# Optimization experiments

Measured on AMD Instinct MI355X. Metric: run time of the kernel, lower is better.

The kernel has to match this reference:

```python
import jax, jax.numpy as jnp
import numpy as np
from jax import lax

N, C, H, W = 16, 512, 64, 64
INTER, HEADS, GROUPS, K = 512, 64, 8, 7
HEAD_DIM = INTER // HEADS


def setup_inputs() -> dict:
    key = jax.random.key(0)
    ks = jax.random.split(key, 12)
    s = 0.02
    return {
        "x": jax.random.normal(ks[0], (N, C, H, W), jnp.float32),
        "conv_w": jax.random.normal(ks[1], (INTER, C // GROUPS, K, K), jnp.float32) * s,
        "conv_b": jax.random.normal(ks[2], (INTER,), jnp.float32) * s,
        "ln_g": jnp.ones((INTER,), jnp.float32),
        "ln_b": jnp.zeros((INTER,), jnp.float32),
        "qw": jax.random.normal(ks[3], (INTER, INTER), jnp.float32) * s,
        "qb": jax.random.normal(ks[4], (INTER,), jnp.float32) * s,
        "kw": jax.random.normal(ks[5], (INTER, INTER), jnp.float32) * s,
        "kb": jax.random.normal(ks[6], (INTER,), jnp.float32) * s,
        "vw": jax.random.normal(ks[7], (INTER, INTER), jnp.float32) * s,
        "vb": jax.random.normal(ks[8], (INTER,), jnp.float32) * s,
        "pw": jax.random.normal(ks[9], (C, INTER), jnp.float32) * s,
        "pb": jax.random.normal(ks[10], (C,), jnp.float32) * s,
        "beta": jax.random.normal(ks[11], (1,), jnp.float32),
    }


def reference(x, conv_w, conv_b, ln_g, ln_b, qw, qb, kw, kb, vw, vb, pw, pb, beta):
    n, c, h, w = x.shape
    hw = h * w
    pad = (K - 1) // 2
    # grouped conv, NCHW
    xc = lax.conv_general_dilated(
        x, conv_w, window_strides=(1, 1), padding=[(pad, pad), (pad, pad)],
        dimension_numbers=("NCHW", "OIHW", "NCHW"), feature_group_count=GROUPS)
    xc = xc + conv_b[None, :, None, None]
    xc = xc.reshape(n, INTER, hw).transpose(0, 2, 1)  # [N, HW, INTER]
    # LayerNorm over channel dim
    mu = jnp.mean(xc, axis=-1, keepdims=True)
    var = jnp.mean(jnp.square(xc - mu), axis=-1, keepdims=True)
    xn = (xc - mu) * lax.rsqrt(var + 1e-5) * ln_g + ln_b
    # projections (torch Linear: y = x @ W.T + b)
    q = (xn @ qw.T + qb).reshape(n, hw, HEADS, HEAD_DIM).transpose(0, 2, 1, 3)  # [N,h,HW,d]
    k = (xn @ kw.T + kb).reshape(n, hw, HEADS, HEAD_DIM).transpose(0, 2, 3, 1)  # [N,h,d,HW]
    v = (xn @ vw.T + vb).reshape(n, hw, HEADS, HEAD_DIM).transpose(0, 2, 1, 3)  # [N,h,HW,d]
    k = jax.nn.softmax(k, axis=3)  # softmax over tokens
    corr = jnp.einsum("nhds,nhse->nhde", k, v)      # [N,h,d,d] compact context
    atten = jnp.einsum("nhsd,nhde->nhse", q, corr)  # [N,h,HW,d]
    atten = atten.transpose(0, 2, 1, 3).reshape(n, hw, INTER)
    xa = (atten @ pw.T + pb).transpose(0, 2, 1).reshape(n, c, h, w)
    return beta[0] * xa + x
```

## Files before the change

kernel.cpp:

```cpp
#include <hip/hip_runtime.h>
#include <hip/hip_bf16.h>

#define N_IMG 16
#define C_DIM 512
#define H_DIM 64
#define W_DIM 64
#define HW 4096
#define INTER 512
#define HEADS 64
#define GROUPS 8
#define KSZ 7
#define CPG 64
#define M_TOT (N_IMG * HW)

typedef short bf16x8 __attribute__((ext_vector_type(8)));
typedef short bf16x4 __attribute__((ext_vector_type(4)));
typedef float f32x4 __attribute__((ext_vector_type(4)));
typedef unsigned int u32;

__device__ __forceinline__ unsigned short f2bf(float f) {
    __hip_bfloat16 h = __float2bfloat16(f);
    return *reinterpret_cast<unsigned short*>(&h);
}
__device__ __forceinline__ float bf2f(unsigned short u) {
    u32 x = ((u32)u) << 16;
    union { u32 i; float f; } c; c.i = x; return c.f;
}
__device__ __forceinline__ void gload16(const void* g, void* l) {
    __builtin_amdgcn_global_load_lds(
        (const __attribute__((address_space(1))) u32*)g,
        (__attribute__((address_space(3))) u32*)l, 16, 0, 0);
}

__global__ __launch_bounds__(256) void zero_kernel(float* __restrict__ p)
{
    p[blockIdx.x * 256 + threadIdx.x] = 0.f;
}

__global__ __launch_bounds__(256) void wpack_kernel(
    const float* __restrict__ cw, unsigned short* __restrict__ pk)
{
    int p = blockIdx.x * 256 + threadIdx.x;
    int ci = p & 63;
    int co = (p >> 6) & 63;
    int r  = p >> 12;
    int dx = r % 7;
    int dyg = r / 7;
    int dy = dyg % 7;
    int g  = dyg / 7;
    float v = cw[(((size_t)(g * 64 + co)) * 64 + ci) * 49 + dy * 7 + dx];
    pk[(size_t)(g * 49 + dy * 7 + dx) * 4096 + co * 64 + (ci ^ ((co & 7) << 3))] = f2bf(v);
}

__global__ __launch_bounds__(256) void wpack_proj_kernel(
    const float* __restrict__ w, unsigned short* __restrict__ wp)
{
    int e = blockIdx.x * 256 + threadIdx.x;
    int j = e & 7;
    int chunk = (e >> 3) & 511;
    int kt = (e >> 12) & 15;
    int t = e >> 16;
    int col = chunk & 127, kq = chunk >> 7;
    wp[e] = f2bf(w[(size_t)(t * 128 + col) * 512 + kt * 32 + kq * 8 + j]);
}

__global__ __launch_bounds__(256) void xprep_kernel(
    const float* __restrict__ x, unsigned short* __restrict__ xb)
{
    const int row = blockIdx.x;
    const int g   = blockIdx.y;
    const int n   = blockIdx.z;
    const int tid = threadIdx.x;
    unsigned short* dst = xb + ((size_t)(n * 8 + g) * 70 + row) * 4608;

    if (row < 3 || row > 66) {
        bf16x8 z = (bf16x8){0,0,0,0,0,0,0,0};
        *(bf16x8*)&dst[tid * 8] = z;
        *(bf16x8*)&dst[(256 + tid) * 8] = z;
        if (tid < 64) *(bf16x8*)&dst[(512 + tid) * 8] = z;
        return;
    }
    const int y = row - 3;
    const int xcol = tid & 63;
    const int oct = tid >> 6;
    const int col = xcol + 3;
    const int cswz = (col & 7) << 3;
    const float* src = x + (((size_t)(n * C_DIM + g * CPG)) * H_DIM + y) * W_DIM + xcol;
#pragma unroll
    for (int h = 0; h < 2; ++h) {
        const int ci0 = oct * 16 + h * 8;
        unsigned short tmp[8];
#pragma unroll
        for (int j = 0; j < 8; ++j)
            tmp[j] = f2bf(src[(size_t)(ci0 + j) * (H_DIM * W_DIM)]);
        *(bf16x8*)&dst[col * 64 + (ci0 ^ cswz)] = *(bf16x8*)tmp;
    }
    if (tid < 64) {
        const int hc[8] = {0, 1, 2, 67, 68, 69, 70, 71};
        int c = hc[tid >> 3], o8 = (tid & 7) * 8;
        *(bf16x8*)&dst[c * 64 + (o8 ^ ((c & 7) << 3))] = (bf16x8){0,0,0,0,0,0,0,0};
    }
}

__global__ __launch_bounds__(256) void conv_mfma2_kernel(
    const unsigned short* __restrict__ xb, const unsigned short* __restrict__ pk,
    const float* __restrict__ cb, unsigned short* __restrict__ xc)
{
    __shared__ __align__(16) unsigned short in_ring[4 * 72 * 64];
    __shared__ __align__(16) unsigned short w_lds[2 * 4096];

    const int bid  = blockIdx.x;
    const int wgid = (bid & 7) * 256 + (bid >> 3);
    const int g  = wgid >> 8;
    const int n  = (wgid >> 4) & 15;
    const int y0 = (wgid & 15) * 4;
    const int tid  = threadIdx.x;
    const int lane = tid & 63;
    const int wv   = tid >> 6;
    const int lx   = lane & 15;
    const int q4   = lane >> 4;
    const int koff = q4 * 8;

    const unsigned short* xbase = xb + ((size_t)(n * 8 + g) * 70) * 4608;
    const unsigned short* pkg   = pk + (size_t)g * 49 * 4096;

    f32x4 acc[4][4];
#pragma unroll
    for (int i = 0; i < 4; ++i)
#pragma unroll
        for (int j = 0; j < 4; ++j) acc[i][j] = (f32x4){0.f, 0.f, 0.f, 0.f};

#pragma unroll
    for (int r = 0; r < 4; ++r) {
        const unsigned short* src = xbase + (size_t)(y0 + r) * 4608;
        gload16(src + tid * 8,         &in_ring[r * 4608 + tid * 8]);
        gload16(src + (256 + tid) * 8, &in_ring[r * 4608 + (256 + tid) * 8]);
        if (tid < 64)
            gload16(src + (512 + tid) * 8, &in_ring[r * 4608 + (512 + tid) * 8]);
    }
    gload16(pkg + tid * 8,         &w_lds[tid * 8]);
    gload16(pkg + (256 + tid) * 8, &w_lds[(256 + tid) * 8]);
    __syncthreads();

    for (int dy = 0; dy < 7; ++dy) {
        if (dy > 0) {
            const int slot = (dy + 3) & 3;
            const unsigned short* src = xbase + (size_t)(y0 + dy + 3) * 4608;
            gload16(src + tid * 8,         &in_ring[slot * 4608 + tid * 8]);
            gload16(src + (256 + tid) * 8, &in_ring[slot * 4608 + (256 + tid) * 8]);
            if (tid < 64)
                gload16(src + (512 + tid) * 8, &in_ring[slot * 4608 + (512 + tid) * 8]);
            __syncthreads();
        }
#pragma unroll
        for (int dx = 0; dx < 7; ++dx) {
            const int t = dy * 7 + dx;
            if (t < 48) {
                const unsigned short* wsrc = pkg + (size_t)(t + 1) * 4096;
                unsigned short* wdst = &w_lds[((t + 1) & 1) * 4096];
                gload16(wsrc + tid * 8,         wdst + tid * 8);
                gload16(wsrc + (256 + tid) * 8, wdst + (256 + tid) * 8);
            }
            const unsigned short* wcur = &w_lds[(t & 1) * 4096];
            bf16x8 b[2][4];
#pragma unroll
            for (int kc = 0; kc < 2; ++kc)
#pragma unroll
                for (int ct = 0; ct < 4; ++ct) {
                    const int co = ct * 16 + lx;
                    b[kc][ct] = *(const bf16x8*)
                        &wcur[co * 64 + ((kc * 32 + koff) ^ ((co & 7) << 3))];
                }
            const int col  = wv * 16 + lx + dx;
            const int cswz = (col & 7) << 3;
#pragma unroll
            for (int ty = 0; ty < 4; ++ty) {
                const int slot = (dy + ty) & 3;
#pragma unroll
                for (int kc = 0; kc < 2; ++kc) {
                    bf16x8 a = *(const bf16x8*)
                        &in_ring[slot * 4608 + col * 64 + ((kc * 32 + koff) ^ cswz)];
#pragma unroll
                    for (int ct = 0; ct < 4; ++ct)
                        acc[ty][ct] = __builtin_amdgcn_mfma_f32_16x16x32_bf16(
                            a, b[kc][ct], acc[ty][ct], 0, 0, 0);
                }
            }
            __syncthreads();
        }
    }

#pragma unroll
    for (int ct = 0; ct < 4; ++ct) {
        const float bv = cb[g * 64 + ct * 16 + lx];
        const int cidx = g * 64 + ct * 16 + lx;
#pragma unroll
        for (int ty = 0; ty < 4; ++ty) {
            const int yy = y0 + ty;
#pragma unroll
            for (int r = 0; r < 4; ++r) {
                const int xx = wv * 16 + q4 * 4 + r;
                xc[((size_t)(n * HW + yy * W_DIM + xx)) * INTER + cidx]
                    = f2bf(acc[ty][ct][r] + bv);
            }
        }
    }
}

__global__ __launch_bounds__(256) void ln_kernel(
    unsigned short* __restrict__ xc, const float* __restrict__ g,
    const float* __restrict__ b)
{
    const int tid  = threadIdx.x;
    const int half = tid >> 7;
    const int l    = tid & 127;
    const size_t row = (size_t)blockIdx.x * 2 + half;

    bf16x4 u = *(const bf16x4*)(xc + row * INTER + l * 4);
    float v0 = bf2f((unsigned short)u[0]), v1 = bf2f((unsigned short)u[1]);
    float v2 = bf2f((unsigned short)u[2]), v3 = bf2f((unsigned short)u[3]);
    float s  = v0 + v1 + v2 + v3;
    float sq = v0 * v0 + v1 * v1 + v2 * v2 + v3 * v3;
#pragma unroll
    for (int off = 32; off; off >>= 1) {
        s  += __shfl_xor(s, off);
        sq += __shfl_xor(sq, off);
    }
    __shared__ float red[4][2];
    const int wid = tid >> 6;
    if ((tid & 63) == 0) { red[wid][0] = s; red[wid][1] = sq; }
    __syncthreads();
    const int w0 = half * 2;
    float S  = red[w0][0] + red[w0 + 1][0];
    float SQ = red[w0][1] + red[w0 + 1][1];
    float mu  = S * (1.f / INTER);
    float var = SQ * (1.f / INTER) - mu * mu;
    float rs  = rsqrtf(var + 1e-5f);
    float4 gg = ((const float4*)g)[l];
    float4 bb = ((const float4*)b)[l];
    bf16x4 o;
    o[0] = (short)f2bf((v0 - mu) * rs * gg.x + bb.x);
    o[1] = (short)f2bf((v1 - mu) * rs * gg.y + bb.y);
    o[2] = (short)f2bf((v2 - mu) * rs * gg.z + bb.z);
    o[3] = (short)f2bf((v3 - mu) * rs * gg.w + bb.w);
    *(bf16x4*)(xc + row * INTER + l * 4) = o;
}

__global__ __launch_bounds__(256, 2) void gemm_kv_corr_kernel(
    const unsigned short* __restrict__ A,
    const unsigned short* __restrict__ Wk, const unsigned short* __restrict__ Wv,
    const float* __restrict__ bk, const float* __restrict__ bv,
    float* __restrict__ crw, float* __restrict__ esw)
{
    __shared__ __align__(16) unsigned short pool[32768];
    unsigned short* ek_lds = pool;
    unsigned short* v_lds  = pool + 16384;

    const int tid  = threadIdx.x;
    const int lane = tid & 63;
    const int w    = tid >> 6;
    const int lx   = lane & 15;
    const int kq4  = lane >> 4;

    const int orig = blockIdx.x;
    const int wgid = (orig & 7) * 256 + (orig >> 3);
    const int m0   = (wgid >> 2) * 128;
    const int ct4  = wgid & 3;
    const int mbase = (w & 1) * 64;
    const int nbase = (w >> 1) * 64;
    const int n = m0 >> 12;

    const unsigned short* wkt = Wk + (size_t)ct4 * 65536;
    const unsigned short* wvt = Wv + (size_t)ct4 * 65536;

    f32x4 acck[4][4], accv[4][4];
#pragma unroll
    for (int i = 0; i < 4; ++i)
#pragma unroll
        for (int j = 0; j < 4; ++j) {
            acck[i][j] = (f32x4){0.f, 0.f, 0.f, 0.f};
            accv[i][j] = (f32x4){0.f, 0.f, 0.f, 0.f};
        }

#pragma unroll
    for (int it = 0; it < 2; ++it) {
        int c = it * 256 + tid;
        gload16(A + (size_t)(m0 + (c & 127)) * 512 + (c >> 7) * 8, &pool[c * 8]);
        gload16(wkt + c * 8, &pool[(1024 + c) * 8]);
        gload16(wvt + c * 8, &pool[(2048 + c) * 8]);
    }
    __syncthreads();

    for (int kt = 0; kt < 16; ++kt) {
        const int b = kt & 1;
        if (kt < 15) {
            const int nb = b ^ 1;
#pragma unroll
            for (int it = 0; it < 2; ++it) {
                int c = it * 256 + tid;
                gload16(A + (size_t)(m0 + (c & 127)) * 512 + (kt + 1) * 32 + (c >> 7) * 8,
                        &pool[(nb * 512 + c) * 8]);
                gload16(wkt + (size_t)(kt + 1) * 4096 + c * 8, &pool[(1024 + nb * 512 + c) * 8]);
                gload16(wvt + (size_t)(kt + 1) * 4096 + c * 8, &pool[(2048 + nb * 512 + c) * 8]);
            }
        }
        bf16x8 a[4], bkf[4], bvf[4];
#pragma unroll
        for (int i = 0; i < 4; ++i) {
            a[i]   = *(const bf16x8*)&pool[(b * 512 + kq4 * 128 + mbase + i * 16 + lx) * 8];
            bkf[i] = *(const bf16x8*)&pool[(1024 + b * 512 + kq4 * 128 + nbase + i * 16 + lx) * 8];
            bvf[i] = *(const bf16x8*)&pool[(2048 + b * 512 + kq4 * 128 + nbase + i * 16 + lx) * 8];
        }
#pragma unroll
        for (int i = 0; i < 4; ++i)
#pragma unroll
            for (int j = 0; j < 4; ++j) {
                acck[i][j] = __builtin_amdgcn_mfma_f32_16x16x32_bf16(a[i], bkf[j], acck[i][j], 0, 0, 0);
                accv[i][j] = __builtin_amdgcn_mfma_f32_16x16x32_bf16(a[i], bvf[j], accv[i][j], 0, 0, 0);
            }
        __syncthreads();
    }

#pragma unroll
    for (int j = 0; j < 4; ++j) {
        const int colk = nbase + j * 16 + lx;
        const float bkv = bk[ct4 * 128 + colk];
        const float bvv = bv[ct4 * 128 + colk];
        const int sw = (colk & 7) << 3;
#pragma unroll
        for (int i = 0; i < 4; ++i) {
            const int t0 = mbase + i * 16 + kq4 * 4;
            const int idx = colk * 128 + (t0 ^ sw);
            bf16x4 ew, vw;
#pragma unroll
            for (int r = 0; r < 4; ++r) {
                ew[r] = (short)f2bf(__expf(acck[i][j][r] + bkv));
                vw[r] = (short)f2bf(accv[i][j][r] + bvv);
            }
            *(bf16x4*)&ek_lds[idx] = ew;
            *(bf16x4*)&v_lds[idx]  = vw;
        }
    }
    const int d = lane >> 3, e = lane & 7;
    const int hbase = (w >> 1) * 8;
#pragma unroll
    for (int h = 0; h < 8; ++h) {
        const int hb = hbase + h;
        const int ck = hb * 8 + d;
        const int ce = hb * 8 + e;
        const int swk = d << 3, swe = e << 3;
        float crh = 0.f, esh = 0.f;
#pragma unroll
        for (int tb = 0; tb < 16; ++tb) {
            const int t0 = mbase + tb * 4;
            bf16x4 ekv = *(const bf16x4*)&ek_lds[ck * 128 + (t0 ^ swk)];
            bf16x4 vvv = *(const bf16x4*)&v_lds[ce * 128 + (t0 ^ swe)];
#pragma unroll
            for (int r = 0; r < 4; ++r) {
                float ekf = bf2f((unsigned short)ekv[r]);
                crh = fmaf(ekf, bf2f((unsigned short)vvv[r]), crh);
                esh += ekf;
            }
        }
        const int nh = n * 64 + ct4 * 16 + hb;
        atomicAdd(&crw[(size_t)nh * 64 + d * 8 + e], crh);
        if (e == 0) atomicAdd(&esw[nh * 8 + d], esh);
    }
}

__global__ __launch_bounds__(256) void norm_corr_kernel(
    const float* __restrict__ crw, const float* __restrict__ esw,
    float* __restrict__ corr)
{
    int idx = blockIdx.x * 256 + threadIdx.x;
    int nh = idx >> 6, d = (idx >> 3) & 7;
    corr[idx] = crw[idx] / esw[nh * 8 + d];
}

__global__ __launch_bounds__(256) void gemm_q_atten_kernel(
    const unsigned short* __restrict__ A, const unsigned short* __restrict__ Wp,
    const float* __restrict__ bias, const float* __restrict__ corr,
    unsigned short* __restrict__ Y)
{
    __shared__ __align__(16) unsigned short pool[24576];
    unsigned short* q_lds = pool;
    float* corr_lds = (float*)(pool + 16384);

    const int tid  = threadIdx.x;
    const int lane = tid & 63;
    const int w    = tid >> 6;
    const int lx   = lane & 15;
    const int kq4  = lane >> 4;

    const int orig = blockIdx.x;
    const int wgid = (orig & 7) * 128 + (orig >> 3);
    const int m0 = (wgid >> 2) * 256;
    const int n0 = (wgid & 3) * 128;
    const int mbase = (w & 1) * 128;
    const int nbase = (w >> 1) * 64;
    const int n = m0 >> 12;

    f32x4 acc[8][4];
#pragma unroll
    for (int i = 0; i < 8; ++i)
#pragma unroll
        for (int j = 0; j < 4; ++j) acc[i][j] = (f32x4){0.f, 0.f, 0.f, 0.f};

    const unsigned short* wpt = Wp + (size_t)(wgid & 3) * 65536;

#pragma unroll
    for (int it = 0; it < 4; ++it) {
        int c = it * 256 + tid;
        gload16(A + (size_t)(m0 + (c & 255)) * 512 + (c >> 8) * 8, &pool[c * 8]);
    }
#pragma unroll
    for (int it = 0; it < 2; ++it) {
        int c = it * 256 + tid;
        gload16(wpt + c * 8, &pool[16384 + c * 8]);
    }
    __syncthreads();

    for (int kt = 0; kt < 16; ++kt) {
        const int b = kt & 1;
        if (kt < 15) {
            const int nb = b ^ 1;
#pragma unroll
            for (int it = 0; it < 4; ++it) {
                int c = it * 256 + tid;
                gload16(A + (size_t)(m0 + (c & 255)) * 512 + (kt + 1) * 32 + (c >> 8) * 8,
                        &pool[(nb * 1024 + c) * 8]);
            }
#pragma unroll
            for (int it = 0; it < 2; ++it) {
                int c = it * 256 + tid;
                gload16(wpt + (size_t)(kt + 1) * 4096 + c * 8,
                        &pool[16384 + (nb * 512 + c) * 8]);
            }
        }
        bf16x8 a[8], bf[4];
#pragma unroll
        for (int i = 0; i < 8; ++i)
            a[i] = *(const bf16x8*)&pool[(b * 1024 + kq4 * 256 + mbase + i * 16 + lx) * 8];
#pragma unroll
        for (int j = 0; j < 4; ++j)
            bf[j] = *(const bf16x8*)&pool[16384 + (b * 512 + kq4 * 128 + nbase + j * 16 + lx) * 8];
#pragma unroll
        for (int i = 0; i < 8; ++i)
#pragma unroll
            for (int j = 0; j < 4; ++j)
                acc[i][j] = __builtin_amdgcn_mfma_f32_16x16x32_bf16(a[i], bf[j], acc[i][j], 0, 0, 0);
        __syncthreads();
    }

    const int h0 = n0 >> 3;
    for (int i = tid; i < 1024; i += 256) {
        int h = i >> 6, de = i & 63;
        corr_lds[h * 68 + de] = corr[((size_t)(n * 64) + h0 + h) * 64 + de];
    }
#pragma unroll
    for (int ch = 0; ch < 2; ++ch) {
#pragma unroll
        for (int j = 0; j < 4; ++j) {
            const int col = nbase + j * 16 + lx;
            const float bvv = bias[n0 + col];
#pragma unroll
            for (int il = 0; il < 4; ++il) {
                const int i = ch * 4 + il;
#pragma unroll
                for (int r = 0; r < 4; ++r) {
                    const int lrow = (w & 1) * 64 + il * 16 + kq4 * 4 + r;
                    q_lds[lrow * 128 + col] = f2bf(acc[i][j][r] + bvv);
                }
            }
        }
        __syncthreads();
#pragma unroll
        for (int rep = 0; rep < 8; ++rep) {
            const int s = rep * 16 + (tid >> 4);
            const int hl = tid & 15;
            bf16x8 q8 = *(const bf16x8*)&q_lds[s * 128 + hl * 8];
            float qf[8];
#pragma unroll
            for (int d = 0; d < 8; ++d) qf[d] = bf2f((unsigned short)q8[d]);
            float o[8] = {};
#pragma unroll
            for (int d = 0; d < 8; ++d) {
                float4 c0 = *(const float4*)&corr_lds[hl * 68 + d * 8];
                float4 c1 = *(const float4*)&corr_lds[hl * 68 + d * 8 + 4];
                o[0] = fmaf(qf[d], c0.x, o[0]); o[1] = fmaf(qf[d], c0.y, o[1]);
                o[2] = fmaf(qf[d], c0.z, o[2]); o[3] = fmaf(qf[d], c0.w, o[3]);
                o[4] = fmaf(qf[d], c1.x, o[4]); o[5] = fmaf(qf[d], c1.y, o[5]);
                o[6] = fmaf(qf[d], c1.z, o[6]); o[7] = fmaf(qf[d], c1.w, o[7]);
            }
            bf16x8 ov;
#pragma unroll
            for (int d = 0; d < 8; ++d) ov[d] = (short)f2bf(o[d]);
            const size_t token = (size_t)m0 + (s >> 6) * 128 + (s & 63) + ch * 64;
            *(bf16x8*)&Y[token * 512 + n0 + hl * 8] = ov;
        }
        if (ch == 0) __syncthreads();
    }
}

__global__ __launch_bounds__(256) void gemm_p_kernel(
    const unsigned short* __restrict__ A, const unsigned short* __restrict__ Wp,
    const float* __restrict__ bias, float* __restrict__ Y,
    const float* __restrict__ xres, const float* __restrict__ betap)
{
    __shared__ __align__(16) unsigned short pool[24576];
    const int tid  = threadIdx.x;
    const int lane = tid & 63;
    const int w    = tid >> 6;
    const int lx   = lane & 15;
    const int kq4  = lane >> 4;

    const int orig = blockIdx.x;
    const int wgid = (orig & 7) * 128 + (orig >> 3);
    const int m0 = (wgid >> 2) * 256;
    const int n0 = (wgid & 3) * 128;
    const int mbase = (w & 1) * 128;
    const int nbase = (w >> 1) * 64;

    f32x4 acc[8][4];
#pragma unroll
    for (int i = 0; i < 8; ++i)
#pragma unroll
        for (int j = 0; j < 4; ++j) acc[i][j] = (f32x4){0.f, 0.f, 0.f, 0.f};

    const unsigned short* wpt = Wp + (size_t)(wgid & 3) * 65536;

#pragma unroll
    for (int it = 0; it < 4; ++it) {
        int c = it * 256 + tid;
        gload16(A + (size_t)(m0 + (c & 255)) * 512 + (c >> 8) * 8, &pool[c * 8]);
    }
#pragma unroll
    for (int it = 0; it < 2; ++it) {
        int c = it * 256 + tid;
        gload16(wpt + c * 8, &pool[16384 + c * 8]);
    }
    __syncthreads();

    for (int kt = 0; kt < 16; ++kt) {
        const int b = kt & 1;
        if (kt < 15) {
            const int nb = b ^ 1;
#pragma unroll
            for (int it = 0; it < 4; ++it) {
                int c = it * 256 + tid;
                gload16(A + (size_t)(m0 + (c & 255)) * 512 + (kt + 1) * 32 + (c >> 8) * 8,
                        &pool[(nb * 1024 + c) * 8]);
            }
#pragma unroll
            for (int it = 0; it < 2; ++it) {
                int c = it * 256 + tid;
                gload16(wpt + (size_t)(kt + 1) * 4096 + c * 8,
                        &pool[16384 + (nb * 512 + c) * 8]);
            }
        }
        bf16x8 a[8], bf[4];
#pragma unroll
        for (int i = 0; i < 8; ++i)
            a[i] = *(const bf16x8*)&pool[(b * 1024 + kq4 * 256 + mbase + i * 16 + lx) * 8];
#pragma unroll
        for (int j = 0; j < 4; ++j)
            bf[j] = *(const bf16x8*)&pool[16384 + (b * 512 + kq4 * 128 + nbase + j * 16 + lx) * 8];
#pragma unroll
        for (int i = 0; i < 8; ++i)
#pragma unroll
            for (int j = 0; j < 4; ++j)
                acc[i][j] = __builtin_amdgcn_mfma_f32_16x16x32_bf16(a[i], bf[j], acc[i][j], 0, 0, 0);
        __syncthreads();
    }

    const float beta = betap[0];
    const int nimg = m0 >> 12;
#pragma unroll
    for (int j = 0; j < 4; ++j) {
        const int c = n0 + nbase + j * 16 + lx;
        const float pbv = bias[c];
        const size_t cbase = ((size_t)(nimg * 512 + c)) * 4096;
#pragma unroll
        for (int i = 0; i < 8; ++i) {
            const int s = (m0 & 4095) + mbase + i * 16 + kq4 * 4;
            float4 xr = *(const float4*)(xres + cbase + s);
            float4 o;
            o.x = beta * (acc[i][j][0] + pbv) + xr.x;
            o.y = beta * (acc[i][j][1] + pbv) + xr.y;
            o.z = beta * (acc[i][j][2] + pbv) + xr.z;
            o.w = beta * (acc[i][j][3] + pbv) + xr.w;
            *(float4*)(Y + cbase + s) = o;
        }
    }
}

extern "C" void kernel_launch(void* const* d_in, const int* in_sizes, int n_in,
                              void* d_out, int out_size, void* d_ws, size_t ws_size,
                              hipStream_t stream)
{
    (void)in_sizes; (void)n_in; (void)out_size; (void)ws_size;
    const float* x   = (const float*)d_in[0];
    const float* cw  = (const float*)d_in[1];
    const float* cb  = (const float*)d_in[2];
    const float* lng = (const float*)d_in[3];
    const float* lnb = (const float*)d_in[4];
    const float* qw  = (const float*)d_in[5];
    const float* qb  = (const float*)d_in[6];
    const float* kw  = (const float*)d_in[7];
    const float* kb  = (const float*)d_in[8];
    const float* vw  = (const float*)d_in[9];
    const float* vb  = (const float*)d_in[10];
    const float* pw  = (const float*)d_in[11];
    const float* pb  = (const float*)d_in[12];
    const float* beta = (const float*)d_in[13];
    float* out = (float*)d_out;

    char* ws = (char*)d_ws;
    const size_t SZ  = (size_t)M_TOT * INTER * sizeof(float);
    const size_t HSZ = (size_t)M_TOT * INTER * 2;
    unsigned short* xc   = (unsigned short*)ws;
    unsigned short* qbuf = (unsigned short*)(ws + HSZ);
    float* crw  = (float*)(ws + SZ);
    float* esw  = crw + 65536;
    float* corr = (float*)(ws + SZ + (1 << 20));
    unsigned short* pk  = (unsigned short*)(ws + SZ + (2 << 20));
    unsigned short* kwb = (unsigned short*)(ws + SZ + (6 << 20));
    unsigned short* vwb = kwb + 262144;
    unsigned short* qwb = vwb + 262144;
    unsigned short* pwb = qwb + 262144;
    unsigned short* xb  = pwb + 262144;

    zero_kernel<<<dim3(288), 256, 0, stream>>>(crw);
    wpack_kernel<<<dim3(6272), 256, 0, stream>>>(cw, pk);
    wpack_proj_kernel<<<dim3(1024), 256, 0, stream>>>(kw, kwb);
    wpack_proj_kernel<<<dim3(1024), 256, 0, stream>>>(vw, vwb);
    wpack_proj_kernel<<<dim3(1024), 256, 0, stream>>>(qw, qwb);
    wpack_proj_kernel<<<dim3(1024), 256, 0, stream>>>(pw, pwb);
    xprep_kernel<<<dim3(70, 8, 16), 256, 0, stream>>>(x, xb);

    conv_mfma2_kernel<<<dim3(2048), 256, 0, stream>>>(xb, pk, cb, xc);
    ln_kernel<<<dim3(M_TOT / 2), 256, 0, stream>>>(xc, lng, lnb);

    gemm_kv_corr_kernel<<<dim3(2048), 256, 0, stream>>>(xc, kwb, vwb, kb, vb, crw, esw);
    norm_corr_kernel<<<dim3(256), 256, 0, stream>>>(crw, esw, corr);
    gemm_q_atten_kernel<<<dim3(1024), 256, 0, stream>>>(xc, qwb, qb, corr, qbuf);
    gemm_p_kernel<<<dim3(1024), 256, 0, stream>>>(qbuf, pwb, pb, out, x, beta);
}
```

Baseline: 583.7 us.

## Fold Q projection, context and output projection into one per-image weight

Because the output is linear in xn once corr is known, the Q projection, the per-head corr multiply and the output projection are composed into a single 512x512 weight per image (Pw·blockdiag(corr)·Qw), plus a per-image bias. This replaces the Q GEMM with its attention epilogue and the separate P GEMM with small weight-composition kernels and one GEMM over the activations. The activation-side GEMM work drops from two passes to one and the intermediate q buffer is no longer written or read. In exchange there are extra small launches, per-image weights to build and pack, and an additional bf16 rounding of the composed weight, which could change accuracy.

After: 522.8 us. 1.12x faster.

```diff
diff --git a/kernel.cpp b/kernel.cpp
--- a/kernel.cpp
+++ b/kernel.cpp
@@ -62,6 +62,13 @@
     int t = e >> 16;
     int col = chunk & 127, kq = chunk >> 7;
     wp[e] = f2bf(w[(size_t)(t * 128 + col) * 512 + kt * 32 + kq * 8 + j]);
+}
+
+__global__ __launch_bounds__(256) void pwcast_kernel(
+    const float* __restrict__ w, unsigned short* __restrict__ wb)
+{
+    int i = blockIdx.x * 256 + threadIdx.x;
+    wb[i] = f2bf(w[i]);
 }
 
 __global__ __launch_bounds__(256) void xprep_kernel(
@@ -377,15 +384,159 @@
     corr[idx] = crw[idx] / esw[nh * 8 + d];
 }
 
-__global__ __launch_bounds__(256) void gemm_q_atten_kernel(
+__global__ __launch_bounds__(256) void gcomp_kernel(
+    const float* __restrict__ qw, const float* __restrict__ corr,
+    unsigned short* __restrict__ G)
+{
+    const int h = blockIdx.x;
+    const int n = blockIdx.y;
+    const int tid = threadIdx.x;
+    __shared__ float C[64];
+    if (tid < 64) C[tid] = corr[((size_t)(n * 64 + h)) * 64 + tid];
+    __syncthreads();
+#pragma unroll
+    for (int rep = 0; rep < 2; ++rep) {
+        const int k = rep * 256 + tid;
+        float o[8] = {};
+#pragma unroll
+        for (int d = 0; d < 8; ++d) {
+            float qv = qw[(size_t)(h * 8 + d) * 512 + k];
+#pragma unroll
+            for (int e = 0; e < 8; ++e) o[e] = fmaf(qv, C[d * 8 + e], o[e]);
+        }
+        bf16x8 ov;
+#pragma unroll
+        for (int e = 0; e < 8; ++e) ov[e] = (short)f2bf(o[e]);
+        *(bf16x8*)&G[((size_t)n * 512 + k) * 512 + h * 8] = ov;
+    }
+}
+
+__global__ __launch_bounds__(256) void compose_kernel(
+    const unsigned short* __restrict__ Pwb, const unsigned short* __restrict__ G,
+    unsigned short* __restrict__ Wf)
+{
+    __shared__ __align__(16) unsigned short pool[16384];
+    const int tid  = threadIdx.x;
+    const int lane = tid & 63;
+    const int w    = tid >> 6;
+    const int lx   = lane & 15;
+    const int kq4  = lane >> 4;
+
+    const int tile = blockIdx.x;
+    const int n    = blockIdx.y;
+    const int m0 = (tile >> 2) * 128;
+    const int n0 = (tile & 3) * 128;
+    const int mbase = (w & 1) * 64;
+    const int nbase = (w >> 1) * 64;
+    const unsigned short* Gn = G + (size_t)n * 262144;
+
+    f32x4 acc[4][4];
+#pragma unroll
+    for (int i = 0; i < 4; ++i)
+#pragma unroll
+        for (int j = 0; j < 4; ++j) acc[i][j] = (f32x4){0.f, 0.f, 0.f, 0.f};
+
+#pragma unroll
+    for (int it = 0; it < 2; ++it) {
+        int c = it * 256 + tid;
+        gload16(Pwb + (size_t)(m0 + (c & 127)) * 512 + (c >> 7) * 8, &pool[c * 8]);
+        gload16(Gn + (size_t)(n0 + (c & 127)) * 512 + (c >> 7) * 8, &pool[(1024 + c) * 8]);
+    }
+    __syncthreads();
+
+    for (int kt = 0; kt < 16; ++kt) {
+        const int b = kt & 1;
+        if (kt < 15) {
+            const int nb = b ^ 1;
+#pragma unroll
+            for (int it = 0; it < 2; ++it) {
+                int c = it * 256 + tid;
+                gload16(Pwb + (size_t)(m0 + (c & 127)) * 512 + (kt + 1) * 32 + (c >> 7) * 8,
+                        &pool[(nb * 512 + c) * 8]);
+                gload16(Gn + (size_t)(n0 + (c & 127)) * 512 + (kt + 1) * 32 + (c >> 7) * 8,
+                        &pool[(1024 + nb * 512 + c) * 8]);
+            }
+        }
+        bf16x8 a[4], bf[4];
+#pragma unroll
+        for (int i = 0; i < 4; ++i) {
+            a[i]  = *(const bf16x8*)&pool[(b * 512 + kq4 * 128 + mbase + i * 16 + lx) * 8];
+            bf[i] = *(const bf16x8*)&pool[(1024 + b * 512 + kq4 * 128 + nbase + i * 16 + lx) * 8];
+        }
+#pragma unroll
+        for (int i = 0; i < 4; ++i)
+#pragma unroll
+            for (int j = 0; j < 4; ++j)
+                acc[i][j] = __builtin_amdgcn_mfma_f32_16x16x32_bf16(a[i], bf[j], acc[i][j], 0, 0, 0);
+        __syncthreads();
+    }
+
+#pragma unroll
+    for (int j = 0; j < 4; ++j) {
+        const int col = n0 + nbase + j * 16 + lx;
+#pragma unroll
+        for (int i = 0; i < 4; ++i) {
+            const int rowb = m0 + mbase + i * 16 + kq4 * 4;
+#pragma unroll
+            for (int r = 0; r < 4; ++r)
+                Wf[(size_t)n * 262144 + (size_t)(rowb + r) * 512 + col] = f2bf(acc[i][j][r]);
+        }
+    }
+}
+
+__global__ __launch_bounds__(256) void wfpack_kernel(
+    const unsigned short* __restrict__ Wf, unsigned short* __restrict__ wfp)
+{
+    const int n = blockIdx.y;
+    int e = blockIdx.x * 256 + threadIdx.x;
+    int j = e & 7;
+    int chunk = (e >> 3) & 511;
+    int kt = (e >> 12) & 15;
+    int t = e >> 16;
+    int col = chunk & 127, kq = chunk >> 7;
+    wfp[(size_t)n * 262144 + e] =
+        Wf[(size_t)n * 262144 + (size_t)(t * 128 + col) * 512 + kt * 32 + kq * 8 + j];
+}
+
+__global__ __launch_bounds__(256) void bias2_kernel(
+    const float* __restrict__ qb, const float* __restrict__ corr,
+    const float* __restrict__ pw, const float* __restrict__ pb,
+    float* __restrict__ b2)
+{
+    const int n = blockIdx.x;
+    const int tid = threadIdx.x;
+    __shared__ float qbc[512];
+#pragma unroll
+    for (int rep = 0; rep < 2; ++rep) {
+        int j = rep * 256 + tid;
+        int h = j >> 3, e = j & 7;
+        float s = 0.f;
+#pragma unroll
+        for (int d = 0; d < 8; ++d)
+            s += qb[h * 8 + d] * corr[((size_t)(n * 64 + h)) * 64 + d * 8 + e];
+        qbc[j] = s;
+    }
+    __syncthreads();
+#pragma unroll
+    for (int rep = 0; rep < 2; ++rep) {
+        int c = rep * 256 + tid;
+        const float4* pr = (const float4*)(pw + (size_t)c * 512);
+        float s = pb[c];
+        for (int q = 0; q < 128; ++q) {
+            float4 pv = pr[q];
+            s += qbc[q * 4 + 0] * pv.x + qbc[q * 4 + 1] * pv.y
+               + qbc[q * 4 + 2] * pv.z + qbc[q * 4 + 3] * pv.w;
+        }
+        b2[n * 512 + c] = s;
+    }
+}
+
+__global__ __launch_bounds__(256) void gemm_p_kernel(
     const unsigned short* __restrict__ A, const unsigned short* __restrict__ Wp,
-    const float* __restrict__ bias, const float* __restrict__ corr,
-    unsigned short* __restrict__ Y)
+    const float* __restrict__ bias, float* __restrict__ Y,
+    const float* __restrict__ xres, const float* __restrict__ betap)
 {
     __shared__ __align__(16) unsigned short pool[24576];
-    unsigned short* q_lds = pool;
-    float* corr_lds = (float*)(pool + 16384);
-
     const int tid  = threadIdx.x;
     const int lane = tid & 63;
     const int w    = tid >> 6;
@@ -398,7 +549,7 @@
     const int n0 = (wgid & 3) * 128;
     const int mbase = (w & 1) * 128;
     const int nbase = (w >> 1) * 64;
-    const int n = m0 >> 12;
+    const int nimg = m0 >> 12;
 
     f32x4 acc[8][4];
 #pragma unroll
@@ -406,7 +557,7 @@
 #pragma unroll
         for (int j = 0; j < 4; ++j) acc[i][j] = (f32x4){0.f, 0.f, 0.f, 0.f};
 
-    const unsigned short* wpt = Wp + (size_t)(wgid & 3) * 65536;
+    const unsigned short* wpt = Wp + (size_t)nimg * 262144 + (size_t)(wgid & 3) * 65536;
 
 #pragma unroll
     for (int it = 0; it < 4; ++it) {
@@ -452,133 +603,11 @@
         __syncthreads();
     }
 
-    const int h0 = n0 >> 3;
-    for (int i = tid; i < 1024; i += 256) {
-        int h = i >> 6, de = i & 63;
-        corr_lds[h * 68 + de] = corr[((size_t)(n * 64) + h0 + h) * 64 + de];
-    }
-#pragma unroll
-    for (int ch = 0; ch < 2; ++ch) {
-#pragma unroll
-        for (int j = 0; j < 4; ++j) {
-            const int col = nbase + j * 16 + lx;
-            const float bvv = bias[n0 + col];
-#pragma unroll
-            for (int il = 0; il < 4; ++il) {
-                const int i = ch * 4 + il;
-#pragma unroll
-                for (int r = 0; r < 4; ++r) {
-                    const int lrow = (w & 1) * 64 + il * 16 + kq4 * 4 + r;
-                    q_lds[lrow * 128 + col] = f2bf(acc[i][j][r] + bvv);
-                }
-            }
-        }
-        __syncthreads();
-#pragma unroll
-        for (int rep = 0; rep < 8; ++rep) {
-            const int s = rep * 16 + (tid >> 4);
-            const int hl = tid & 15;
-            bf16x8 q8 = *(const bf16x8*)&q_lds[s * 128 + hl * 8];
-            float qf[8];
-#pragma unroll
-            for (int d = 0; d < 8; ++d) qf[d] = bf2f((unsigned short)q8[d]);
-            float o[8] = {};
-#pragma unroll
-            for (int d = 0; d < 8; ++d) {
-                float4 c0 = *(const float4*)&corr_lds[hl * 68 + d * 8];
-                float4 c1 = *(const float4*)&corr_lds[hl * 68 + d * 8 + 4];
-                o[0] = fmaf(qf[d], c0.x, o[0]); o[1] = fmaf(qf[d], c0.y, o[1]);
-                o[2] = fmaf(qf[d], c0.z, o[2]); o[3] = fmaf(qf[d], c0.w, o[3]);
-                o[4] = fmaf(qf[d], c1.x, o[4]); o[5] = fmaf(qf[d], c1.y, o[5]);
-                o[6] = fmaf(qf[d], c1.z, o[6]); o[7] = fmaf(qf[d], c1.w, o[7]);
-            }
-            bf16x8 ov;
-#pragma unroll
-            for (int d = 0; d < 8; ++d) ov[d] = (short)f2bf(o[d]);
-            const size_t token = (size_t)m0 + (s >> 6) * 128 + (s & 63) + ch * 64;
-            *(bf16x8*)&Y[token * 512 + n0 + hl * 8] = ov;
-        }
-        if (ch == 0) __syncthreads();
-    }
-}
-
-__global__ __launch_bounds__(256) void gemm_p_kernel(
-    const unsigned short* __restrict__ A, const unsigned short* __restrict__ Wp,
-    const float* __restrict__ bias, float* __restrict__ Y,
-    const float* __restrict__ xres, const float* __restrict__ betap)
-{
-    __shared__ __align__(16) unsigned short pool[24576];
-    const int tid  = threadIdx.x;
-    const int lane = tid & 63;
-    const int w    = tid >> 6;
-    const int lx   = lane & 15;
-    const int kq4  = lane >> 4;
-
-    const int orig = blockIdx.x;
-    const int wgid = (orig & 7) * 128 + (orig >> 3);
-    const int m0 = (wgid >> 2) * 256;
-    const int n0 = (wgid & 3) * 128;
-    const int mbase = (w & 1) * 128;
-    const int nbase = (w >> 1) * 64;
-
-    f32x4 acc[8][4];
-#pragma unroll
-    for (int i = 0; i < 8; ++i)
-#pragma unroll
-        for (int j = 0; j < 4; ++j) acc[i][j] = (f32x4){0.f, 0.f, 0.f, 0.f};
-
-    const unsigned short* wpt = Wp + (size_t)(wgid & 3) * 65536;
-
-#pragma unroll
-    for (int it = 0; it < 4; ++it) {
-        int c = it * 256 + tid;
-        gload16(A + (size_t)(m0 + (c & 255)) * 512 + (c >> 8) * 8, &pool[c * 8]);
-    }
-#pragma unroll
-    for (int it = 0; it < 2; ++it) {
-        int c = it * 256 + tid;
-        gload16(wpt + c * 8, &pool[16384 + c * 8]);
-    }
-    __syncthreads();
-
-    for (int kt = 0; kt < 16; ++kt) {
-        const int b = kt & 1;
-        if (kt < 15) {
-            const int nb = b ^ 1;
-#pragma unroll
-            for (int it = 0; it < 4; ++it) {
-                int c = it * 256 + tid;
-                gload16(A + (size_t)(m0 + (c & 255)) * 512 + (kt + 1) * 32 + (c >> 8) * 8,
-                        &pool[(nb * 1024 + c) * 8]);
-            }
-#pragma unroll
-            for (int it = 0; it < 2; ++it) {
-                int c = it * 256 + tid;
-                gload16(wpt + (size_t)(kt + 1) * 4096 + c * 8,
-                        &pool[16384 + (nb * 512 + c) * 8]);
-            }
-        }
-        bf16x8 a[8], bf[4];
-#pragma unroll
-        for (int i = 0; i < 8; ++i)
-            a[i] = *(const bf16x8*)&pool[(b * 1024 + kq4 * 256 + mbase + i * 16 + lx) * 8];
-#pragma unroll
-        for (int j = 0; j < 4; ++j)
-            bf[j] = *(const bf16x8*)&pool[16384 + (b * 512 + kq4 * 128 + nbase + j * 16 + lx) * 8];
-#pragma unroll
-        for (int i = 0; i < 8; ++i)
-#pragma unroll
-            for (int j = 0; j < 4; ++j)
-                acc[i][j] = __builtin_amdgcn_mfma_f32_16x16x32_bf16(a[i], bf[j], acc[i][j], 0, 0, 0);
-        __syncthreads();
-    }
-
     const float beta = betap[0];
-    const int nimg = m0 >> 12;
 #pragma unroll
     for (int j = 0; j < 4; ++j) {
         const int c = n0 + nbase + j * 16 + lx;
-        const float pbv = bias[c];
+        const float pbv = bias[nimg * 512 + c];
         const size_t cbase = ((size_t)(nimg * 512 + c)) * 4096;
 #pragma unroll
         for (int i = 0; i < 8; ++i) {
@@ -619,23 +648,24 @@
     const size_t SZ  = (size_t)M_TOT * INTER * sizeof(float);
     const size_t HSZ = (size_t)M_TOT * INTER * 2;
     unsigned short* xc   = (unsigned short*)ws;
-    unsigned short* qbuf = (unsigned short*)(ws + HSZ);
+    unsigned short* G    = (unsigned short*)(ws + HSZ);
+    unsigned short* wfin = G + (size_t)16 * 262144;
+    unsigned short* wfp  = wfin + (size_t)16 * 262144;
+    unsigned short* pwb  = wfp + (size_t)16 * 262144;
+    float* b2            = (float*)(pwb + 262144);
     float* crw  = (float*)(ws + SZ);
     float* esw  = crw + 65536;
     float* corr = (float*)(ws + SZ + (1 << 20));
     unsigned short* pk  = (unsigned short*)(ws + SZ + (2 << 20));
     unsigned short* kwb = (unsigned short*)(ws + SZ + (6 << 20));
     unsigned short* vwb = kwb + 262144;
-    unsigned short* qwb = vwb + 262144;
-    unsigned short* pwb = qwb + 262144;
-    unsigned short* xb  = pwb + 262144;
+    unsigned short* xb  = vwb + 262144;
 
     zero_kernel<<<dim3(288), 256, 0, stream>>>(crw);
     wpack_kernel<<<dim3(6272), 256, 0, stream>>>(cw, pk);
     wpack_proj_kernel<<<dim3(1024), 256, 0, stream>>>(kw, kwb);
     wpack_proj_kernel<<<dim3(1024), 256, 0, stream>>>(vw, vwb);
-    wpack_proj_kernel<<<dim3(1024), 256, 0, stream>>>(qw, qwb);
-    wpack_proj_kernel<<<dim3(1024), 256, 0, stream>>>(pw, pwb);
+    pwcast_kernel<<<dim3(1024), 256, 0, stream>>>(pw, pwb);
     xprep_kernel<<<dim3(70, 8, 16), 256, 0, stream>>>(x, xb);
 
     conv_mfma2_kernel<<<dim3(2048), 256, 0, stream>>>(xb, pk, cb, xc);
@@ -643,6 +673,11 @@
 
     gemm_kv_corr_kernel<<<dim3(2048), 256, 0, stream>>>(xc, kwb, vwb, kb, vb, crw, esw);
     norm_corr_kernel<<<dim3(256), 256, 0, stream>>>(crw, esw, corr);
-    gemm_q_atten_kernel<<<dim3(1024), 256, 0, stream>>>(xc, qwb, qb, corr, qbuf);
-    gemm_p_kernel<<<dim3(1024), 256, 0, stream>>>(qbuf, pwb, pb, out, x, beta);
-}
+
+    gcomp_kernel<<<dim3(64, 16), 256, 0, stream>>>(qw, corr, G);
+    compose_kernel<<<dim3(16, 16), 256, 0, stream>>>(pwb, G, wfin);
+    wfpack_kernel<<<dim3(1024, 16), 256, 0, stream>>>(wfin, wfp);
+    bias2_kernel<<<dim3(16), 256, 0, stream>>>(qb, corr, pw, pb, b2);
+
+    gemm_p_kernel<<<dim3(1024), 256, 0, stream>>>(xc, wfp, b2, out, x, beta);
+}
```
